# Kernel tuning notes

Hardware: AMD Instinct MI355X
Metric: run time of the kernel (lower is better)

## Reference

```python
import jax, jax.numpy as jnp
from jax import lax
import numpy as np

BETA = 0.5
ITERATION = 50
K = 1
EPS = 1e-5  # F.normalize eps


def cost_matrix_cosine(x, y):
    # x: [b,m,d], y: [b,n,d] -> cosine distance [b,m,n]
    xn = x / jnp.maximum(jnp.linalg.norm(x, axis=-1, keepdims=True), EPS)
    yn = y / jnp.maximum(jnp.linalg.norm(y, axis=-1, keepdims=True), EPS)
    return 1.0 - jnp.einsum('bmd,bnd->bmn', xn, yn)


def ipot(C, x_len, x_pad, y_len, y_pad, joint_pad, beta, iteration, k):
    # C: [b,m,n]; x_*: txt (m); y_*: img (n). Returns transport plan [b,m,n].
    b, m, n = C.shape
    jp_t = jnp.transpose(joint_pad, (0, 2, 1))                      # [b,n,m]
    A = jnp.where(jp_t, 0.0, jnp.exp(-jnp.transpose(C, (0, 2, 1)) / beta))
    T0 = jnp.where(jp_t, 0.0, 1.0)                                  # [b,n,m]
    sigma0 = jnp.where(x_pad, 0.0, 1.0 / x_len[:, None])[:, :, None]  # [b,m,1]
    x_mask = (x_pad.astype(C.dtype) * 1e4)[:, None, :]              # [b,1,m]
    y_mask = (y_pad.astype(C.dtype) * 1e4)[:, None, :]              # [b,1,n]
    xl = x_len[:, None, None]
    yl = y_len[:, None, None]

    def outer(carry, _):
        T, sigma = carry
        Q = A * T                                                   # [b,n,m]
        def inner(sig, _):
            # sig: [b,m,1]
            delta = 1.0 / (yl * jnp.transpose(jnp.matmul(Q, sig), (0, 2, 1)) + y_mask)  # [b,1,n]
            sig = jnp.transpose(1.0 / (xl * jnp.matmul(delta, Q) + x_mask), (0, 2, 1))  # [b,m,1]
            return sig, delta
        sigma, deltas = lax.scan(inner, sigma, None, length=k)
        delta = deltas[-1]                                          # [b,1,n]
        T = jnp.transpose(delta, (0, 2, 1)) * Q * jnp.transpose(sigma, (0, 2, 1))  # [b,n,m]
        return (T, sigma), None

    (T, _), _ = lax.scan(outer, (T0, sigma0), None, length=iteration)
    return jnp.transpose(T, (0, 2, 1))                              # [b,m,n]


def optimal_transport_dist(txt_emb, img_emb, txt_pad, img_pad):
    cost = cost_matrix_cosine(txt_emb, img_emb)                     # [b,m,n]
    joint_pad = txt_pad[:, :, None] | img_pad[:, None, :]           # [b,m,n]
    cost = jnp.where(joint_pad, 0.0, cost)
    txt_len = (txt_pad.shape[1] - jnp.sum(txt_pad, axis=1)).astype(cost.dtype)
    img_len = (img_pad.shape[1] - jnp.sum(img_pad, axis=1)).astype(cost.dtype)
    T = ipot(lax.stop_gradient(cost), txt_len, txt_pad, img_len, img_pad,
             joint_pad, BETA, ITERATION, K)
    # trace(cost @ T^T) == sum_ij cost_ij * plan_ij, per sample
    return jnp.sum(cost * lax.stop_gradient(T), axis=(1, 2))        # [b]


def reference(entitytxt_vec, object_vec, entitytxt_num, object_num):
    txt_nodes_emb = entitytxt_vec.astype(jnp.float32)               # [b,tl,d]
    img_nodes_emb = object_vec[:, 1:].astype(jnp.float32)           # [b,il,d]
    txt_pad = entitytxt_num == 0                                    # [b,tl] bool
    img_pad = object_num[:, 1:] == 0                                # [b,il] bool
    ot_dist = optimal_transport_dist(txt_nodes_emb, img_nodes_emb, txt_pad, img_pad)
    ot_loss = jnp.sum(ot_dist) * 0.01
    return ot_loss


def setup_inputs():
    key = jax.random.key(0)
    k1, k2, k3, k4 = jax.random.split(key, 4)
    b, tl, il1, d = 256, 128, 128, 1024
    entitytxt_vec = jax.random.normal(k1, (b, tl, d), dtype=jnp.float32)
    object_vec = jax.random.normal(k2, (b, il1, d), dtype=jnp.float32)
    entitytxt_num = jax.random.randint(k3, (b, tl), 0, 2, dtype=jnp.int32)
    object_num = jax.random.randint(k4, (b, il1), 0, 2, dtype=jnp.int32)
    # guarantee at least one valid node per sample (avoid 1/0 lengths)
    entitytxt_num = entitytxt_num.at[:, 0].set(1)
    object_num = object_num.at[:, 1].set(1)
    return {"entitytxt_vec": entitytxt_vec, "object_vec": object_vec,
            "entitytxt_num": entitytxt_num, "object_num": object_num}
```

## Files before the change

kernel.cpp:

```cpp
#include <hip/hip_runtime.h>
#include <math.h>

#define BATCH 256
#define M 128
#define NIMG 127
#define NP 128
#define D 1024
#define BK 64
#define NT (D / BK)
#define ITERS 50
#define LROW 72
#define ASTRIDE 132
#define NTHREADS 1024
#define NWAVES 16

typedef __attribute__((ext_vector_type(8))) short bf16x8;
typedef __attribute__((ext_vector_type(4))) float floatx4;

static __device__ __forceinline__ unsigned pack_bf16x2(float a, float b) {
    unsigned ua = __builtin_bit_cast(unsigned, a);
    unsigned ub = __builtin_bit_cast(unsigned, b);
    ua += 0x7fffu + ((ua >> 16) & 1u);
    ub += 0x7fffu + ((ub >> 16) & 1u);
    return (ua >> 16) | (ub & 0xffff0000u);
}

template<int CTRL>
static __device__ __forceinline__ float dpp_add(float v) {
    int s = __builtin_amdgcn_update_dpp(0, __builtin_bit_cast(int, v), CTRL, 0xf, 0xf, true);
    return v + __builtin_bit_cast(float, s);
}
static __device__ __forceinline__ float red16(float v) {
    v = dpp_add<0x121>(v);
    v = dpp_add<0x122>(v);
    v = dpp_add<0x124>(v);
    v = dpp_add<0x128>(v);
    return v;
}

static __device__ __forceinline__ void barrier_lgkm() {
    asm volatile("s_waitcnt lgkmcnt(0)" ::: "memory");
    __builtin_amdgcn_s_barrier();
    __builtin_amdgcn_sched_barrier(0);
}

static __device__ __forceinline__ void load_tile(const float* __restrict__ xb,
                                                 const float* __restrict__ yb,
                                                 int kk, int r0, int c16,
                                                 float4 (&vx)[2], float4 (&vy)[2]) {
#pragma unroll
    for (int it = 0; it < 2; ++it) {
        const int r = r0 + it * 64;
        vx[it] = *(const float4*)(xb + (size_t)r * D + kk + c16 * 4);
        float4 z = make_float4(0.f, 0.f, 0.f, 0.f);
        if (r < NIMG) z = *(const float4*)(yb + (size_t)r * D + kk + c16 * 4);
        vy[it] = z;
    }
}

static __device__ __forceinline__ void stage_tile(short* __restrict__ Xs, short* __restrict__ Ys,
                                                  int r0, int c16,
                                                  const float4 (&vx)[2], const float4 (&vy)[2],
                                                  float (&ssx)[2], float (&ssy)[2]) {
#pragma unroll
    for (int it = 0; it < 2; ++it) {
        const int r = r0 + it * 64;
        float4 v = vx[it];
        ssx[it] = fmaf(v.x, v.x, fmaf(v.y, v.y, fmaf(v.z, v.z, fmaf(v.w, v.w, ssx[it]))));
        uint2 p;
        p.x = pack_bf16x2(v.x, v.y);
        p.y = pack_bf16x2(v.z, v.w);
        *(uint2*)(&Xs[r * LROW + c16 * 4]) = p;
        v = vy[it];
        ssy[it] = fmaf(v.x, v.x, fmaf(v.y, v.y, fmaf(v.z, v.z, fmaf(v.w, v.w, ssy[it]))));
        p.x = pack_bf16x2(v.x, v.y);
        p.y = pack_bf16x2(v.z, v.w);
        *(uint2*)(&Ys[r * LROW + c16 * 4]) = p;
    }
}

static __device__ __forceinline__ void mfma_tile(const short* __restrict__ Xs,
                                                 const short* __restrict__ Ys,
                                                 int mbase, int nbase, int col, int quad,
                                                 floatx4 (&acc)[2][2]) {
#pragma unroll
    for (int ks = 0; ks < 2; ++ks) {
        const int koff = ks * 32 + quad * 8;
        bf16x8 af[2], bfr[2];
#pragma unroll
        for (int tr = 0; tr < 2; ++tr)
            af[tr] = *(const bf16x8*)(&Xs[(mbase + tr * 16 + col) * LROW + koff]);
#pragma unroll
        for (int tc = 0; tc < 2; ++tc)
            bfr[tc] = *(const bf16x8*)(&Ys[(nbase + tc * 16 + col) * LROW + koff]);
#pragma unroll
        for (int tr = 0; tr < 2; ++tr)
#pragma unroll
            for (int tc = 0; tc < 2; ++tc)
                acc[tr][tc] = __builtin_amdgcn_mfma_f32_16x16x32_bf16(
                    af[tr], bfr[tc], acc[tr][tc], 0, 0, 0);
    }
}

__launch_bounds__(NTHREADS, 1)
__global__ void fused_kernel(const float* __restrict__ xg,
                             const float* __restrict__ yg,
                             const int* __restrict__ xnum,
                             const int* __restrict__ ynum,
                             float* __restrict__ out)
{
    __shared__ __align__(16) unsigned char smem[2 * M * LROW * 2 * sizeof(short)];
    __shared__ __align__(16) float partCS[NWAVES * 128];
    __shared__ __align__(16) float sdelta[NP];
    __shared__ __align__(16) float sxmask[M];
    __shared__ __align__(16) float symask[NP];
    __shared__ __align__(16) float sinvx[M];
    __shared__ __align__(16) float sinvy[NP];
    __shared__ float sxl_s, syl_s;
    __shared__ unsigned scnt[2 * NWAVES];
    __shared__ float swsum[NWAVES];

    short (*Xs)[M * LROW] = reinterpret_cast<short (*)[M * LROW]>(smem);
    short (*Ys)[M * LROW] = reinterpret_cast<short (*)[M * LROW]>(smem + 2 * M * LROW * sizeof(short));
    float* Alds = reinterpret_cast<float*>(smem);

    const int b    = blockIdx.x;
    const int t    = threadIdx.x;
    const int lane = t & 63;
    const int w    = t >> 6;
    const int tj   = t & 15;
    const int i0   = (t >> 4) * 2;
    const int j0   = tj * 8;

    bool tpad = true, ipad = true;
    if (t < M)  { tpad = (xnum[b * M + t] == 0); sxmask[t] = tpad ? 1e4f : 0.0f; }
    if (t < NP) { ipad = !(t < NIMG && ynum[b * 128 + t + 1] != 0); symask[t] = ipad ? 1e4f : 0.0f; }
    unsigned long long bx = __ballot(t < M  && !tpad);
    unsigned long long by = __ballot(t < NP && !ipad);
    if (lane == 0) { scnt[w] = (unsigned)__popcll(bx); scnt[NWAVES + w] = (unsigned)__popcll(by); }
    __syncthreads();
    if (t == 0) {
        float xl = 0.f, yl = 0.f;
        for (int k = 0; k < NWAVES; ++k) { xl += scnt[k]; yl += scnt[NWAVES + k]; }
        sxl_s = xl; syl_s = yl;
    }

    const float* xb = xg + (size_t)b * M * D;
    const float* yb = yg + ((size_t)b * 128 + 1) * D;

    const int r0  = t >> 4;
    const int c16 = t & 15;

    floatx4 acc[2][2];
#pragma unroll
    for (int a = 0; a < 2; ++a)
#pragma unroll
        for (int c = 0; c < 2; ++c) acc[a][c] = (floatx4)0.0f;

    float ssx[2] = {0.f, 0.f};
    float ssy[2] = {0.f, 0.f};

    const int mbase = (w & 3) * 32;
    const int nbase = (w >> 2) * 32;
    const int col   = lane & 15;
    const int quad  = lane >> 4;

    float4 vxa[2], vya[2], vxb[2], vyb[2];
    load_tile(xb, yb, 0,  r0, c16, vxa, vya);
    load_tile(xb, yb, BK, r0, c16, vxb, vyb);
    __syncthreads();

#pragma unroll 1
    for (int ii = 0; ii < NT; ii += 2) {
        stage_tile(Xs[0], Ys[0], r0, c16, vxa, vya, ssx, ssy);
        if (ii + 2 < NT) load_tile(xb, yb, (ii + 2) * BK, r0, c16, vxa, vya);
        barrier_lgkm();
        mfma_tile(Xs[0], Ys[0], mbase, nbase, col, quad, acc);
        stage_tile(Xs[1], Ys[1], r0, c16, vxb, vyb, ssx, ssy);
        if (ii + 3 < NT) load_tile(xb, yb, (ii + 3) * BK, r0, c16, vxb, vyb);
        barrier_lgkm();
        mfma_tile(Xs[1], Ys[1], mbase, nbase, col, quad, acc);
    }

#pragma unroll
    for (int it = 0; it < 2; ++it) {
        ssx[it] = red16(ssx[it]);
        ssy[it] = red16(ssy[it]);
    }
    if (c16 == 0) {
#pragma unroll
        for (int it = 0; it < 2; ++it) {
            const int r = r0 + it * 64;
            sinvx[r] = 1.0f / fmaxf(sqrtf(ssx[it]), 1e-5f);
            sinvy[r] = 1.0f / fmaxf(sqrtf(ssy[it]), 1e-5f);
        }
    }
    barrier_lgkm();

#pragma unroll
    for (int tr = 0; tr < 2; ++tr)
#pragma unroll
        for (int tc = 0; tc < 2; ++tc) {
            const int n = nbase + tc * 16 + col;
            const float ivy_n = sinvy[n];
            const float ymf   = symask[n];
#pragma unroll
            for (int reg = 0; reg < 4; ++reg) {
                const int m = mbase + tr * 16 + quad * 4 + reg;
                const float p = acc[tr][tc][reg] * sinvx[m] * ivy_n;
                const float a = (sxmask[m] + ymf > 0.0f) ? 0.0f : expf(2.0f * p - 2.0f);
                Alds[m * ASTRIDE + n] = a;
            }
        }
    barrier_lgkm();

    const float xl = sxl_s, yl = syl_s;

    float xm[2], ym[8];
    xm[0] = sxmask[i0]; xm[1] = sxmask[i0 + 1];
    *(float4*)ym       = *(const float4*)(&symask[j0]);
    *(float4*)(ym + 4) = *(const float4*)(&symask[j0 + 4]);

    float sn[2];
#pragma unroll
    for (int r = 0; r < 2; ++r)
        sn[r] = (xm[r] > 0.0f) ? 0.0f : __builtin_amdgcn_rcpf(xl);

    float Af[2][8], Q[2][8];
#pragma unroll
    for (int r = 0; r < 2; ++r) {
        float4 a0 = *(const float4*)(&Alds[(i0 + r) * ASTRIDE + j0]);
        float4 a1 = *(const float4*)(&Alds[(i0 + r) * ASTRIDE + j0 + 4]);
        Af[r][0] = a0.x; Af[r][1] = a0.y; Af[r][2] = a0.z; Af[r][3] = a0.w;
        Af[r][4] = a1.x; Af[r][5] = a1.y; Af[r][6] = a1.z; Af[r][7] = a1.w;
#pragma unroll
        for (int j = 0; j < 8; ++j) Q[r][j] = Af[r][j];
    }
    __syncthreads();

    float lp = 0.0f;
    for (int itn = 0; itn < ITERS; ++itn) {
        float cp[8] = {0.f,0.f,0.f,0.f,0.f,0.f,0.f,0.f};
#pragma unroll
        for (int r = 0; r < 2; ++r)
#pragma unroll
            for (int j = 0; j < 8; ++j)
                cp[j] = fmaf(sn[r], Q[r][j], cp[j]);
#pragma unroll
        for (int j = 0; j < 8; ++j) {
            cp[j] += __shfl_xor(cp[j], 16);
            cp[j] += __shfl_xor(cp[j], 32);
        }
        if (lane < 16) {
            float4 c0 = make_float4(cp[0], cp[1], cp[2], cp[3]);
            float4 c1 = make_float4(cp[4], cp[5], cp[6], cp[7]);
            *(float4*)(&partCS[w * 128 + j0])     = c0;
            *(float4*)(&partCS[w * 128 + j0 + 4]) = c1;
        }
        __syncthreads();
        if (t < NP) {
            float s = 0.f;
#pragma unroll
            for (int w8 = 0; w8 < NWAVES; ++w8) s += partCS[w8 * 128 + t];
            sdelta[t] = __builtin_amdgcn_rcpf(yl * s + symask[t]);
        }
        __syncthreads();
        float dl[8];
        *(float4*)dl       = *(const float4*)(&sdelta[j0]);
        *(float4*)(dl + 4) = *(const float4*)(&sdelta[j0 + 4]);
        float rp[2] = {0.f, 0.f};
#pragma unroll
        for (int r = 0; r < 2; ++r)
#pragma unroll
            for (int j = 0; j < 8; ++j)
                rp[r] = fmaf(dl[j], Q[r][j], rp[r]);
#pragma unroll
        for (int r = 0; r < 2; ++r) rp[r] = red16(rp[r]);
#pragma unroll
        for (int r = 0; r < 2; ++r) rp[r] = __shfl(rp[r], lane & 48);
#pragma unroll
        for (int r = 0; r < 2; ++r)
            sn[r] = __builtin_amdgcn_rcpf(xl * rp[r] + xm[r]);

        if (itn < ITERS - 1) {
#pragma unroll
            for (int r = 0; r < 2; ++r) {
                const float f = sn[r];
#pragma unroll
                for (int j = 0; j < 8; ++j)
                    Q[r][j] *= Af[r][j] * dl[j] * f;
            }
        } else {
#pragma unroll
            for (int r = 0; r < 2; ++r)
#pragma unroll
                for (int j = 0; j < 8; ++j) {
                    const float a = Af[r][j];
                    if (a > 0.0f)
                        lp = fmaf(-0.5f * logf(a) * dl[j] * sn[r], Q[r][j], lp);
                }
        }
    }

#pragma unroll
    for (int off = 32; off > 0; off >>= 1) lp += __shfl_down(lp, off);
    if (lane == 0) swsum[w] = lp;
    __syncthreads();
    if (t == 0) {
        float tot = 0.f;
        for (int k = 0; k < NWAVES; ++k) tot += swsum[k];
        atomicAdd(out, 0.01f * tot);
    }
}

extern "C" void kernel_launch(void* const* d_in, const int* in_sizes, int n_in,
                              void* d_out, int out_size, void* d_ws, size_t ws_size,
                              hipStream_t stream) {
    const float* x  = (const float*)d_in[0];
    const float* y  = (const float*)d_in[1];
    const int*   xn = (const int*)d_in[2];
    const int*   yn = (const int*)d_in[3];
    float* out = (float*)d_out;
    (void)d_ws; (void)ws_size;

    (void)hipMemsetAsync(out, 0, (size_t)out_size * sizeof(float), stream);
    fused_kernel<<<dim3(BATCH), dim3(NTHREADS), 0, stream>>>(x, y, xn, yn, out);
}
```

Before: 372.4 us.

## Load MFMA operands directly from global memory, bypassing LDS staging

Replaces the LDS-staged bf16 tile pipeline with per-lane direct global loads of the exact fp32 fragments each wave needs for its MFMA operands. The loads are double-buffered in registers and converted to bf16 in place, and the row norms are computed only by the waves that own each row. This removes the LDS writes and reads and the per-tile barriers, adding only an occasional barrier to keep waves roughly in step. In exchange each input row is fetched by four waves instead of once, so global and L2 traffic goes up, and the access pattern is less coalesced (32-byte chunks per lane across rows).

Result: slower. 423.2 us (+13.7%).

```diff
diff --git a/kernel.cpp b/kernel.cpp
--- a/kernel.cpp
+++ b/kernel.cpp
@@ -6,13 +6,11 @@
 #define NIMG 127
 #define NP 128
 #define D 1024
-#define BK 64
-#define NT (D / BK)
 #define ITERS 50
-#define LROW 72
 #define ASTRIDE 132
 #define NTHREADS 1024
 #define NWAVES 16
+#define NHALF 32
 
 typedef __attribute__((ext_vector_type(8))) short bf16x8;
 typedef __attribute__((ext_vector_type(4))) float floatx4;
@@ -25,6 +23,23 @@
     return (ua >> 16) | (ub & 0xffff0000u);
 }
 
+static __device__ __forceinline__ bf16x8 pack8(const float4& a, const float4& b) {
+    union { unsigned u[4]; bf16x8 v; } r;
+    r.u[0] = pack_bf16x2(a.x, a.y);
+    r.u[1] = pack_bf16x2(a.z, a.w);
+    r.u[2] = pack_bf16x2(b.x, b.y);
+    r.u[3] = pack_bf16x2(b.z, b.w);
+    return r.v;
+}
+
+static __device__ __forceinline__ float sq8(const float4& a, const float4& b, float s) {
+    s = fmaf(a.x, a.x, s); s = fmaf(a.y, a.y, s);
+    s = fmaf(a.z, a.z, s); s = fmaf(a.w, a.w, s);
+    s = fmaf(b.x, b.x, s); s = fmaf(b.y, b.y, s);
+    s = fmaf(b.z, b.z, s); s = fmaf(b.w, b.w, s);
+    return s;
+}
+
 template<int CTRL>
 static __device__ __forceinline__ float dpp_add(float v) {
     int s = __builtin_amdgcn_update_dpp(0, __builtin_bit_cast(int, v), CTRL, 0xf, 0xf, true);
@@ -38,68 +53,42 @@
     return v;
 }
 
-static __device__ __forceinline__ void barrier_lgkm() {
-    asm volatile("s_waitcnt lgkmcnt(0)" ::: "memory");
-    __builtin_amdgcn_s_barrier();
-    __builtin_amdgcn_sched_barrier(0);
-}
-
-static __device__ __forceinline__ void load_tile(const float* __restrict__ xb,
-                                                 const float* __restrict__ yb,
-                                                 int kk, int r0, int c16,
-                                                 float4 (&vx)[2], float4 (&vy)[2]) {
-#pragma unroll
-    for (int it = 0; it < 2; ++it) {
-        const int r = r0 + it * 64;
-        vx[it] = *(const float4*)(xb + (size_t)r * D + kk + c16 * 4);
-        float4 z = make_float4(0.f, 0.f, 0.f, 0.f);
-        if (r < NIMG) z = *(const float4*)(yb + (size_t)r * D + kk + c16 * 4);
-        vy[it] = z;
-    }
-}
-
-static __device__ __forceinline__ void stage_tile(short* __restrict__ Xs, short* __restrict__ Ys,
-                                                  int r0, int c16,
-                                                  const float4 (&vx)[2], const float4 (&vy)[2],
-                                                  float (&ssx)[2], float (&ssy)[2]) {
-#pragma unroll
-    for (int it = 0; it < 2; ++it) {
-        const int r = r0 + it * 64;
-        float4 v = vx[it];
-        ssx[it] = fmaf(v.x, v.x, fmaf(v.y, v.y, fmaf(v.z, v.z, fmaf(v.w, v.w, ssx[it]))));
-        uint2 p;
-        p.x = pack_bf16x2(v.x, v.y);
-        p.y = pack_bf16x2(v.z, v.w);
-        *(uint2*)(&Xs[r * LROW + c16 * 4]) = p;
-        v = vy[it];
-        ssy[it] = fmaf(v.x, v.x, fmaf(v.y, v.y, fmaf(v.z, v.z, fmaf(v.w, v.w, ssy[it]))));
-        p.x = pack_bf16x2(v.x, v.y);
-        p.y = pack_bf16x2(v.z, v.w);
-        *(uint2*)(&Ys[r * LROW + c16 * 4]) = p;
-    }
-}
-
-static __device__ __forceinline__ void mfma_tile(const short* __restrict__ Xs,
-                                                 const short* __restrict__ Ys,
-                                                 int mbase, int nbase, int col, int quad,
-                                                 floatx4 (&acc)[2][2]) {
-#pragma unroll
-    for (int ks = 0; ks < 2; ++ks) {
-        const int koff = ks * 32 + quad * 8;
-        bf16x8 af[2], bfr[2];
-#pragma unroll
-        for (int tr = 0; tr < 2; ++tr)
-            af[tr] = *(const bf16x8*)(&Xs[(mbase + tr * 16 + col) * LROW + koff]);
-#pragma unroll
-        for (int tc = 0; tc < 2; ++tc)
-            bfr[tc] = *(const bf16x8*)(&Ys[(nbase + tc * 16 + col) * LROW + koff]);
-#pragma unroll
-        for (int tr = 0; tr < 2; ++tr)
-#pragma unroll
-            for (int tc = 0; tc < 2; ++tc)
-                acc[tr][tc] = __builtin_amdgcn_mfma_f32_16x16x32_bf16(
-                    af[tr], bfr[tc], acc[tr][tc], 0, 0, 0);
-    }
+struct HalfBuf { float4 x0a, x0b, x1a, x1b, y0a, y0b, y1a, y1b; };
+
+static __device__ __forceinline__ void load_half(HalfBuf& hb,
+                                                 const float* __restrict__ xr0,
+                                                 const float* __restrict__ xr1,
+                                                 const float* __restrict__ yr0,
+                                                 const float* __restrict__ yr1,
+                                                 int h) {
+    const int o = h * 32;
+    hb.x0a = *(const float4*)(xr0 + o); hb.x0b = *(const float4*)(xr0 + o + 4);
+    hb.x1a = *(const float4*)(xr1 + o); hb.x1b = *(const float4*)(xr1 + o + 4);
+    hb.y0a = *(const float4*)(yr0 + o); hb.y0b = *(const float4*)(yr0 + o + 4);
+    hb.y1a = *(const float4*)(yr1 + o); hb.y1b = *(const float4*)(yr1 + o + 4);
+}
+
+static __device__ __forceinline__ void proc_half(const HalfBuf& hb, bool yv0, bool yv1,
+                                                 bool doX, bool doY,
+                                                 floatx4 (&acc)[2][2],
+                                                 float& ssx0, float& ssx1,
+                                                 float& ssy0, float& ssy1) {
+    const float4 z = make_float4(0.f, 0.f, 0.f, 0.f);
+    float4 ya0 = yv0 ? hb.y0a : z, yb0 = yv0 ? hb.y0b : z;
+    float4 ya1 = yv1 ? hb.y1a : z, yb1 = yv1 ? hb.y1b : z;
+
+    if (doX) { ssx0 = sq8(hb.x0a, hb.x0b, ssx0); ssx1 = sq8(hb.x1a, hb.x1b, ssx1); }
+    if (doY) { ssy0 = sq8(ya0, yb0, ssy0);       ssy1 = sq8(ya1, yb1, ssy1); }
+
+    bf16x8 af0 = pack8(hb.x0a, hb.x0b);
+    bf16x8 af1 = pack8(hb.x1a, hb.x1b);
+    bf16x8 bf0 = pack8(ya0, yb0);
+    bf16x8 bf1 = pack8(ya1, yb1);
+
+    acc[0][0] = __builtin_amdgcn_mfma_f32_16x16x32_bf16(af0, bf0, acc[0][0], 0, 0, 0);
+    acc[0][1] = __builtin_amdgcn_mfma_f32_16x16x32_bf16(af0, bf1, acc[0][1], 0, 0, 0);
+    acc[1][0] = __builtin_amdgcn_mfma_f32_16x16x32_bf16(af1, bf0, acc[1][0], 0, 0, 0);
+    acc[1][1] = __builtin_amdgcn_mfma_f32_16x16x32_bf16(af1, bf1, acc[1][1], 0, 0, 0);
 }
 
 __launch_bounds__(NTHREADS, 1)
@@ -109,7 +98,7 @@
                              const int* __restrict__ ynum,
                              float* __restrict__ out)
 {
-    __shared__ __align__(16) unsigned char smem[2 * M * LROW * 2 * sizeof(short)];
+    __shared__ __align__(16) float Alds[M * ASTRIDE];
     __shared__ __align__(16) float partCS[NWAVES * 128];
     __shared__ __align__(16) float sdelta[NP];
     __shared__ __align__(16) float sxmask[M];
@@ -120,10 +109,6 @@
     __shared__ unsigned scnt[2 * NWAVES];
     __shared__ float swsum[NWAVES];
 
-    short (*Xs)[M * LROW] = reinterpret_cast<short (*)[M * LROW]>(smem);
-    short (*Ys)[M * LROW] = reinterpret_cast<short (*)[M * LROW]>(smem + 2 * M * LROW * sizeof(short));
-    float* Alds = reinterpret_cast<float*>(smem);
-
     const int b    = blockIdx.x;
     const int t    = threadIdx.x;
     const int lane = t & 63;
@@ -145,11 +130,19 @@
         sxl_s = xl; syl_s = yl;
     }
 
+    const int wm = w & 3, wn = w >> 2;
+    const int col = lane & 15, quad = lane >> 4;
+    const int mbase = wm * 32, nbase = wn * 32;
+
     const float* xb = xg + (size_t)b * M * D;
     const float* yb = yg + ((size_t)b * 128 + 1) * D;
 
-    const int r0  = t >> 4;
-    const int c16 = t & 15;
+    const float* xr0 = xb + (size_t)(mbase + col) * D + quad * 8;
+    const float* xr1 = xb + (size_t)(mbase + 16 + col) * D + quad * 8;
+    const int yi0 = nbase + col, yi1 = nbase + 16 + col;
+    const bool yv0 = (yi0 < NIMG), yv1 = (yi1 < NIMG);
+    const float* yr0 = yb + (size_t)(yv0 ? yi0 : 0) * D + quad * 8;
+    const float* yr1 = yb + (size_t)(yv1 ? yi1 : 0) * D + quad * 8;
 
     floatx4 acc[2][2];
 #pragma unroll
@@ -157,45 +150,40 @@
 #pragma unroll
         for (int c = 0; c < 2; ++c) acc[a][c] = (floatx4)0.0f;
 
-    float ssx[2] = {0.f, 0.f};
-    float ssy[2] = {0.f, 0.f};
-
-    const int mbase = (w & 3) * 32;
-    const int nbase = (w >> 2) * 32;
-    const int col   = lane & 15;
-    const int quad  = lane >> 4;
-
-    float4 vxa[2], vya[2], vxb[2], vyb[2];
-    load_tile(xb, yb, 0,  r0, c16, vxa, vya);
-    load_tile(xb, yb, BK, r0, c16, vxb, vyb);
-    __syncthreads();
+    float ssx0 = 0.f, ssx1 = 0.f, ssy0 = 0.f, ssy1 = 0.f;
+    const bool doX = (wn == 0);
+    const bool doY = (wm == 0);
+
+    HalfBuf A, B;
+    load_half(A, xr0, xr1, yr0, yr1, 0);
+    load_half(B, xr0, xr1, yr0, yr1, 1);
 
 #pragma unroll 1
-    for (int ii = 0; ii < NT; ii += 2) {
-        stage_tile(Xs[0], Ys[0], r0, c16, vxa, vya, ssx, ssy);
-        if (ii + 2 < NT) load_tile(xb, yb, (ii + 2) * BK, r0, c16, vxa, vya);
-        barrier_lgkm();
-        mfma_tile(Xs[0], Ys[0], mbase, nbase, col, quad, acc);
-        stage_tile(Xs[1], Ys[1], r0, c16, vxb, vyb, ssx, ssy);
-        if (ii + 3 < NT) load_tile(xb, yb, (ii + 3) * BK, r0, c16, vxb, vyb);
-        barrier_lgkm();
-        mfma_tile(Xs[1], Ys[1], mbase, nbase, col, quad, acc);
-    }
-
-#pragma unroll
-    for (int it = 0; it < 2; ++it) {
-        ssx[it] = red16(ssx[it]);
-        ssy[it] = red16(ssy[it]);
-    }
-    if (c16 == 0) {
-#pragma unroll
-        for (int it = 0; it < 2; ++it) {
-            const int r = r0 + it * 64;
-            sinvx[r] = 1.0f / fmaxf(sqrtf(ssx[it]), 1e-5f);
-            sinvy[r] = 1.0f / fmaxf(sqrtf(ssy[it]), 1e-5f);
-        }
-    }
-    barrier_lgkm();
+    for (int hh = 0; hh < NHALF; hh += 2) {
+        proc_half(A, yv0, yv1, doX, doY, acc, ssx0, ssx1, ssy0, ssy1);
+        if (hh + 2 < NHALF) load_half(A, xr0, xr1, yr0, yr1, hh + 2);
+        proc_half(B, yv0, yv1, doX, doY, acc, ssx0, ssx1, ssy0, ssy1);
+        if (hh + 3 < NHALF) load_half(B, xr0, xr1, yr0, yr1, hh + 3);
+        if ((hh & 6) == 6) __builtin_amdgcn_s_barrier();
+    }
+
+    if (doX) {
+        float v0 = ssx0; v0 += __shfl_xor(v0, 16); v0 += __shfl_xor(v0, 32);
+        float v1 = ssx1; v1 += __shfl_xor(v1, 16); v1 += __shfl_xor(v1, 32);
+        if (quad == 0) {
+            sinvx[mbase + col]      = 1.0f / fmaxf(sqrtf(v0), 1e-5f);
+            sinvx[mbase + 16 + col] = 1.0f / fmaxf(sqrtf(v1), 1e-5f);
+        }
+    }
+    if (doY) {
+        float v0 = ssy0; v0 += __shfl_xor(v0, 16); v0 += __shfl_xor(v0, 32);
+        float v1 = ssy1; v1 += __shfl_xor(v1, 16); v1 += __shfl_xor(v1, 32);
+        if (quad == 0) {
+            sinvy[nbase + col]      = 1.0f / fmaxf(sqrtf(v0), 1e-5f);
+            sinvy[nbase + 16 + col] = 1.0f / fmaxf(sqrtf(v1), 1e-5f);
+        }
+    }
+    __syncthreads();
 
 #pragma unroll
     for (int tr = 0; tr < 2; ++tr)
@@ -212,7 +200,7 @@
                 Alds[m * ASTRIDE + n] = a;
             }
         }
-    barrier_lgkm();
+    __syncthreads();
 
     const float xl = sxl_s, yl = syl_s;
 
```
